# Performance work log

Hardware: AMD Instinct MI355X
Metric: run time of the kernel (lower is better)

Reference implementation:

```python
import jax, jax.numpy as jnp
import numpy as np

N = 50000
E = 800000
H = 128

def _mlp_init(key, sizes, bias_flags):
    ws = []
    for i, (din, dout) in enumerate(zip(sizes[:-1], sizes[1:])):
        key, k1, k2 = jax.random.split(key, 3)
        lim = 1.0 / np.sqrt(din)
        W = jax.random.uniform(k1, (din, dout), jnp.float32, -lim, lim)
        ws.append(W)
        if bias_flags[i]:
            ws.append(jax.random.uniform(k2, (dout,), jnp.float32, -lim, lim))
    return key, ws

def setup_inputs() -> dict:
    key = jax.random.key(0)
    key, kh, kx, ke = jax.random.split(key, 4)
    h = jax.random.normal(kh, (N, H), jnp.float32)
    x = jax.random.normal(kx, (N, 3), jnp.float32)
    edge_index = jax.random.randint(ke, (2, E), 0, N, jnp.int64)
    # edge_mlp: Linear(2H+1, H), Linear(H, H), both with bias
    key, (W_e1, b_e1, W_e2, b_e2) = _mlp_init(key, [2 * H + 1, H, H], [True, True])
    # coord_mlp: Linear(H, H) with bias, Linear(H, 1) no bias
    key, (W_c1, b_c1, W_c2) = _mlp_init(key, [H, H, 1], [True, False])
    # node_mlp: Linear(2H, H), Linear(H, H), both with bias
    key, (W_n1, b_n1, W_n2, b_n2) = _mlp_init(key, [2 * H, H, H], [True, True])
    ln_g = jnp.ones((H,), jnp.float32)
    ln_b = jnp.zeros((H,), jnp.float32)
    return {"h": h, "x": x, "edge_index": edge_index,
            "W_e1": W_e1, "b_e1": b_e1, "W_e2": W_e2, "b_e2": b_e2,
            "W_c1": W_c1, "b_c1": b_c1, "W_c2": W_c2,
            "W_n1": W_n1, "b_n1": b_n1, "W_n2": W_n2, "b_n2": b_n2,
            "ln_g": ln_g, "ln_b": ln_b}

def reference(h, x, edge_index, W_e1, b_e1, W_e2, b_e2, W_c1, b_c1, W_c2,
              W_n1, b_n1, W_n2, b_n2, ln_g, ln_b):
    row, col = edge_index[0], edge_index[1]
    coord_diff = x[row] - x[col]                       # [E, 3]
    dist = jnp.linalg.norm(coord_diff, axis=1, keepdims=True)  # [E, 1]
    radial = dist ** 2
    edge_input = jnp.concatenate([h[row], h[col], radial], axis=1)  # [E, 2H+1]
    m_ij = jax.nn.silu(jax.nn.silu(edge_input @ W_e1 + b_e1) @ W_e2 + b_e2)  # [E, H]
    force_scalar = jnp.tanh(jax.nn.silu(m_ij @ W_c1 + b_c1) @ W_c2) * 0.1    # [E, 1]
    norm_diff = coord_diff / (dist + 1e-8)
    force_vector = norm_diff * force_scalar            # [E, 3]
    x_new = x + jax.ops.segment_sum(force_vector, row, num_segments=N)
    m_i = jax.ops.segment_sum(m_ij, row, num_segments=N)  # [N, H]
    node_input = jnp.concatenate([h, m_i], axis=1)     # [N, 2H]
    h_res = h + jax.nn.silu(node_input @ W_n1 + b_n1) @ W_n2 + b_n2
    mu = jnp.mean(h_res, axis=-1, keepdims=True)
    var = jnp.var(h_res, axis=-1, keepdims=True)
    h_new = (h_res - mu) / jnp.sqrt(var + 1e-5) * ln_g + ln_b
    return (h_new, x_new)
```

## Files before the change

kernel.cpp:

```cpp
#include <hip/hip_runtime.h>
#include <hip/hip_bf16.h>

#define NN 50000
#define NE 800000
#define HH 128
#define SCAN_NB 196

typedef short s16x8 __attribute__((ext_vector_type(8)));
typedef float f32x4 __attribute__((ext_vector_type(4)));
typedef unsigned int u32x4 __attribute__((ext_vector_type(4)));
typedef unsigned int u32x2 __attribute__((ext_vector_type(2)));
typedef __bf16 bf16x2 __attribute__((ext_vector_type(2)));

__device__ __forceinline__ float u2f(unsigned int v) {
    float f;
    __builtin_memcpy(&f, &v, 4);
    return f;
}
__device__ __forceinline__ float bf2f(unsigned short u) {
    return u2f(((unsigned int)u) << 16);
}
__device__ __forceinline__ unsigned short f2bf_sw(float f) {
    unsigned int x;
    __builtin_memcpy(&x, &f, 4);
    unsigned int r = (x + 0x7fffu + ((x >> 16) & 1u)) >> 16;
    return (unsigned short)r;
}
__device__ __forceinline__ unsigned int f2bf_pk(float a, float b) {
#if __has_builtin(__builtin_amdgcn_cvt_pk_bf16_f32)
    bf16x2 p = __builtin_amdgcn_cvt_pk_bf16_f32(a, b);
    unsigned int u;
    __builtin_memcpy(&u, &p, 4);
    return u;
#else
    return (unsigned int)f2bf_sw(a) | ((unsigned int)f2bf_sw(b) << 16);
#endif
}
__device__ __forceinline__ unsigned short f2bf(float a) {
#if __has_builtin(__builtin_amdgcn_cvt_pk_bf16_f32)
    return (unsigned short)(f2bf_pk(a, a) & 0xffffu);
#else
    return f2bf_sw(a);
#endif
}
__device__ __forceinline__ float silu(float v) {
    return v * __builtin_amdgcn_rcpf(1.f + __expf(-v));
}

__global__ void prep_kernel(
    const float* __restrict__ W_e1, const float* __restrict__ W_e2,
    const float* __restrict__ W_c1, const float* __restrict__ W_n1,
    const float* __restrict__ W_n2, const int* __restrict__ eidx,
    unsigned short* __restrict__ PWT, unsigned short* __restrict__ W2T,
    unsigned short* __restrict__ Wc1T, unsigned short* __restrict__ Wn1T,
    unsigned short* __restrict__ Wn2T, int* __restrict__ counts) {
    int idx = blockIdx.x * 256 + threadIdx.x;
    if (idx < 32768) {
        int cp = idx >> 7, k = idx & 127;
        int srow = (cp < 128) ? k : (128 + k);
        PWT[idx] = f2bf(W_e1[srow * 128 + (cp & 127)]);
    } else if (idx < 49152) {
        int i = idx - 32768, n = i >> 7, k = i & 127;
        W2T[i] = f2bf(W_e2[k * 128 + n]);
    } else if (idx < 65536) {
        int i = idx - 49152, n = i >> 7, k = i & 127;
        Wc1T[i] = f2bf(W_c1[k * 128 + n]);
    } else if (idx < 98304) {
        int i = idx - 65536, n = i >> 8, k = i & 255;
        Wn1T[i] = f2bf(W_n1[k * 128 + n]);
    } else if (idx < 114688) {
        int i = idx - 98304, n = i >> 7, k = i & 127;
        Wn2T[i] = f2bf(W_n2[k * 128 + n]);
    } else if (idx < 114688 + NE) {
        int e = idx - 114688;
        int r = eidx[e];
        r = r < 0 ? 0 : (r >= NN ? NN - 1 : r);
        atomicAdd(&counts[r], 1);
    }
}

__global__ void k_partial(const int* __restrict__ counts, int* __restrict__ partials) {
    __shared__ int sm[256];
    int idx = blockIdx.x * 256 + threadIdx.x;
    sm[threadIdx.x] = idx < NN ? counts[idx] : 0;
    __syncthreads();
    for (int s = 128; s > 0; s >>= 1) {
        if (threadIdx.x < s) sm[threadIdx.x] += sm[threadIdx.x + s];
        __syncthreads();
    }
    if (threadIdx.x == 0) partials[blockIdx.x] = sm[0];
}
__global__ void k_scanp(const int* __restrict__ partials, int* __restrict__ scanp) {
    __shared__ int sm[256];
    int t = threadIdx.x;
    int v = t < SCAN_NB ? partials[t] : 0;
    sm[t] = v;
    __syncthreads();
    for (int d = 1; d < 256; d <<= 1) {
        int add = t >= d ? sm[t - d] : 0;
        __syncthreads();
        sm[t] += add;
        __syncthreads();
    }
    scanp[t] = sm[t] - v;
}
__global__ void k_offsets(const int* __restrict__ counts, const int* __restrict__ scanp,
                          int* __restrict__ offsets) {
    __shared__ int sm[256];
    int t = threadIdx.x, idx = blockIdx.x * 256 + t;
    int v = idx < NN ? counts[idx] : 0;
    sm[t] = v;
    __syncthreads();
    for (int d = 1; d < 256; d <<= 1) {
        int add = t >= d ? sm[t - d] : 0;
        __syncthreads();
        sm[t] += add;
        __syncthreads();
    }
    if (idx < NN) offsets[idx] = sm[t] - v + scanp[blockIdx.x];
}

__global__ void k_fill(const int* __restrict__ eidx, const int* __restrict__ offsets,
                       int* __restrict__ cursor, unsigned int* __restrict__ rc) {
    int e = blockIdx.x * 256 + threadIdx.x;
    if (e >= NE) return;
    int r = eidx[e];
    int c = eidx[NE + e];
    r = r < 0 ? 0 : (r >= NN ? NN - 1 : r);
    c = c < 0 ? 0 : (c >= NN ? NN - 1 : c);
    int slot = offsets[r] + atomicAdd(&cursor[r], 1);
    rc[slot] = (unsigned int)r | ((unsigned int)c << 16);
}

__global__ __launch_bounds__(256, 4) void pgemm(
    const float* __restrict__ h, const unsigned short* __restrict__ PWT,
    const float* __restrict__ b1,
    float* __restrict__ P1, unsigned short* __restrict__ P2b) {
    __shared__ unsigned short Alds[64 * 136];
    const int tid = threadIdx.x;
    const int n0 = blockIdx.x * 64;

#pragma unroll
    for (int j = 0; j < 4; j++) {
        int idx = tid + j * 256;
        int e = idx >> 4, ch = idx & 15;
        int node = n0 + e;
        if (node >= NN) node = NN - 1;
        const f32x4* p = (const f32x4*)&h[node * 128 + ch * 8];
        f32x4 a = p[0], b = p[1];
        u32x4 s;
        s[0] = f2bf_pk(a[0], a[1]);
        s[1] = f2bf_pk(a[2], a[3]);
        s[2] = f2bf_pk(b[0], b[1]);
        s[3] = f2bf_pk(b[2], b[3]);
        *(u32x4*)&Alds[e * 136 + ch * 8] = s;
    }
    __syncthreads();

    const int lane = tid & 63;
    const int w = tid >> 6;
    const int ln15 = lane & 15;
    const int q8 = (lane >> 4) * 8, q4 = (lane >> 4) * 4;
    const int cbase = w * 64;

    f32x4 acc[4][4];
#pragma unroll
    for (int et = 0; et < 4; et++)
#pragma unroll
        for (int nt = 0; nt < 4; nt++) acc[et][nt] = (f32x4){0.f, 0.f, 0.f, 0.f};
#pragma unroll
    for (int kk = 0; kk < 4; kk++) {
        int k0 = kk * 32 + q8;
        s16x8 a[4], b[4];
#pragma unroll
        for (int et = 0; et < 4; et++)
            a[et] = *(const s16x8*)&Alds[(et * 16 + ln15) * 136 + k0];
#pragma unroll
        for (int nt = 0; nt < 4; nt++)
            b[nt] = *(const s16x8*)&PWT[(cbase + nt * 16 + ln15) * 128 + k0];
#pragma unroll
        for (int et = 0; et < 4; et++)
#pragma unroll
            for (int nt = 0; nt < 4; nt++)
                acc[et][nt] = __builtin_amdgcn_mfma_f32_16x16x32_bf16(
                    b[nt], a[et], acc[et][nt], 0, 0, 0);
    }
#pragma unroll
    for (int nt = 0; nt < 4; nt++) {
        int cp4 = cbase + nt * 16 + q4;
        bool top = cp4 < 128;
        int col4 = cp4 & 127;
        f32x4 badd = top ? *(const f32x4*)&b1[col4] : (f32x4){0.f, 0.f, 0.f, 0.f};
#pragma unroll
        for (int et = 0; et < 4; et++) {
            int node = n0 + et * 16 + ln15;
            if (node >= NN) node = NN - 1;
            f32x4 v;
#pragma unroll
            for (int r = 0; r < 4; r++) v[r] = acc[et][nt][r] + badd[r];
            if (top) {
                *(f32x4*)&P1[(size_t)node * 128 + col4] = v;
            } else {
                u32x2 s;
                s[0] = f2bf_pk(v[0], v[1]);
                s[1] = f2bf_pk(v[2], v[3]);
                *(u32x2*)&P2b[(size_t)node * 128 + col4] = s;
            }
        }
    }
}

__global__ __launch_bounds__(256, 4) void edge_kernel(
    const float* __restrict__ P1, const unsigned short* __restrict__ P2b,
    const float* __restrict__ x, const unsigned int* __restrict__ rc,
    const float* __restrict__ W1full,
    const unsigned short* __restrict__ W2T, const float* __restrict__ b2,
    const unsigned short* __restrict__ Wc1T, const float* __restrict__ bc1,
    const float* __restrict__ wc2,
    float* __restrict__ m_i, float* __restrict__ x_acc) {
    __shared__ unsigned short mid1[64 * 132];
    __shared__ float wls[128];
    __shared__ float rad[64], ndx[64], ndy[64], ndz[64], fsum[64];
    __shared__ int rowA[64], colA[64];

    const int tid = threadIdx.x;
    const int nwg = NE / 64;
    const int qq = nwg >> 3, r8 = nwg & 7;
    const int xcd = blockIdx.x & 7, pos = blockIdx.x >> 3;
    const int swz = (xcd < r8 ? xcd * (qq + 1) : r8 * (qq + 1) + (xcd - r8) * qq) + pos;
    const int e0 = swz * 64;

    if (tid < 64) {
        unsigned int pk = rc[e0 + tid];
        int r = pk & 0xffff, c = pk >> 16;
        rowA[tid] = r; colA[tid] = c;
        float dx = x[r * 3 + 0] - x[c * 3 + 0];
        float dy = x[r * 3 + 1] - x[c * 3 + 1];
        float dz = x[r * 3 + 2] - x[c * 3 + 2];
        float d2 = dx * dx + dy * dy + dz * dz;
        float dist = sqrtf(d2);
        float inv = __builtin_amdgcn_rcpf(dist + 1e-8f);
        rad[tid] = d2;
        ndx[tid] = dx * inv; ndy[tid] = dy * inv; ndz[tid] = dz * inv;
        fsum[tid] = 0.f;
    } else if (tid >= 128 && tid < 256) {
        int c = tid - 128;
        wls[c] = W1full[256 * 128 + c];
    }
    __syncthreads();

#pragma unroll
    for (int j = 0; j < 4; j++) {
        int idx = tid + j * 256;
        int e = idx >> 4, ch = idx & 15;
        int r = rowA[e], c = colA[e];
        const f32x4* q1 = (const f32x4*)&P1[(size_t)r * 128 + ch * 8];
        f32x4 a0 = q1[0], a1 = q1[1];
        u32x4 c01 = *(const u32x4*)&P2b[(size_t)c * 128 + ch * 8];
        float rd = rad[e];
        int colb = ch * 8;
        u32x4 s;
#pragma unroll
        for (int t = 0; t < 2; t++) {
            float v0 = a0[t * 2]     + u2f(c01[t] << 16)         + rd * wls[colb + t * 2];
            float v1 = a0[t * 2 + 1] + u2f(c01[t] & 0xffff0000u) + rd * wls[colb + t * 2 + 1];
            s[t] = f2bf_pk(silu(v0), silu(v1));
        }
#pragma unroll
        for (int t = 0; t < 2; t++) {
            int cc = colb + 4 + t * 2;
            float v0 = a1[t * 2]     + u2f(c01[t + 2] << 16)         + rd * wls[cc];
            float v1 = a1[t * 2 + 1] + u2f(c01[t + 2] & 0xffff0000u) + rd * wls[cc + 1];
            s[t + 2] = f2bf_pk(silu(v0), silu(v1));
        }
        *(u32x4*)&mid1[e * 132 + colb] = s;
    }
    __syncthreads();

    const int lane = tid & 63;
    const int w = tid >> 6;
    const int ln15 = lane & 15;
    const int q8 = (lane >> 4) * 8, q4 = (lane >> 4) * 4;
    const int nbase = w * 32;

    f32x4 acc[4][2];

#pragma unroll
    for (int et = 0; et < 4; et++)
#pragma unroll
        for (int nt = 0; nt < 2; nt++) acc[et][nt] = (f32x4){0.f, 0.f, 0.f, 0.f};
#pragma unroll
    for (int kk = 0; kk < 4; kk++) {
        int k0 = kk * 32 + q8;
        s16x8 a[4], b[2];
#pragma unroll
        for (int et = 0; et < 4; et++)
            a[et] = *(const s16x8*)&mid1[(et * 16 + ln15) * 132 + k0];
#pragma unroll
        for (int nt = 0; nt < 2; nt++)
            b[nt] = *(const s16x8*)&W2T[(nbase + nt * 16 + ln15) * 128 + k0];
#pragma unroll
        for (int et = 0; et < 4; et++)
#pragma unroll
            for (int nt = 0; nt < 2; nt++)
                acc[et][nt] = __builtin_amdgcn_mfma_f32_16x16x32_bf16(
                    b[nt], a[et], acc[et][nt], 0, 0, 0);
    }
    __syncthreads();
    unsigned short* mid2 = mid1;
#pragma unroll
    for (int et = 0; et < 4; et++) {
        int edge = et * 16 + ln15;
#pragma unroll
        for (int nt = 0; nt < 2; nt++) {
            int colb4 = nbase + nt * 16 + q4;
            f32x4 bias = *(const f32x4*)&b2[colb4];
            u32x2 s;
            s[0] = f2bf_pk(silu(acc[et][nt][0] + bias[0]),
                           silu(acc[et][nt][1] + bias[1]));
            s[1] = f2bf_pk(silu(acc[et][nt][2] + bias[2]),
                           silu(acc[et][nt][3] + bias[3]));
            *(u32x2*)&mid2[edge * 132 + colb4] = s;
        }
    }
    __syncthreads();

#pragma unroll
    for (int et = 0; et < 4; et++)
#pragma unroll
        for (int nt = 0; nt < 2; nt++) acc[et][nt] = (f32x4){0.f, 0.f, 0.f, 0.f};
#pragma unroll
    for (int kk = 0; kk < 4; kk++) {
        int k0 = kk * 32 + q8;
        s16x8 a[4], b[2];
#pragma unroll
        for (int et = 0; et < 4; et++)
            a[et] = *(const s16x8*)&mid2[(et * 16 + ln15) * 132 + k0];
#pragma unroll
        for (int nt = 0; nt < 2; nt++)
            b[nt] = *(const s16x8*)&Wc1T[(nbase + nt * 16 + ln15) * 128 + k0];
#pragma unroll
        for (int et = 0; et < 4; et++)
#pragma unroll
            for (int nt = 0; nt < 2; nt++)
                acc[et][nt] = __builtin_amdgcn_mfma_f32_16x16x32_bf16(
                    b[nt], a[et], acc[et][nt], 0, 0, 0);
    }

    {
        int cp2 = (tid & 63) * 2;
        int g = tid >> 6;
        int r0g = g * 16;
        float a0 = 0.f, a1 = 0.f;
        int cur = rowA[r0g];
        for (int row = r0g; row < r0g + 16; row++) {
            int rn = rowA[row];
            if (rn != cur) {
                atomicAdd(&m_i[(size_t)cur * 128 + cp2], a0);
                atomicAdd(&m_i[(size_t)cur * 128 + cp2 + 1], a1);
                a0 = 0.f; a1 = 0.f;
                cur = rn;
            }
            unsigned int v = *(const unsigned int*)&mid2[row * 132 + cp2];
            a0 += u2f(v << 16);
            a1 += u2f(v & 0xffff0000u);
        }
        atomicAdd(&m_i[(size_t)cur * 128 + cp2], a0);
        atomicAdd(&m_i[(size_t)cur * 128 + cp2 + 1], a1);
    }

    {
#pragma unroll
        for (int et = 0; et < 4; et++) {
            float p = 0.f;
#pragma unroll
            for (int nt = 0; nt < 2; nt++) {
                int colb4 = nbase + nt * 16 + q4;
                f32x4 bias = *(const f32x4*)&bc1[colb4];
                f32x4 w2v  = *(const f32x4*)&wc2[colb4];
#pragma unroll
                for (int r = 0; r < 4; r++)
                    p += silu(acc[et][nt][r] + bias[r]) * w2v[r];
            }
            p += __shfl_xor(p, 16, 64);
            p += __shfl_xor(p, 32, 64);
            if ((lane >> 4) == 0) atomicAdd(&fsum[et * 16 + ln15], p);
        }
    }
    __syncthreads();
    if (tid < 64) {
        float fs = tanhf(fsum[tid]) * 0.1f;
        ndx[tid] *= fs; ndy[tid] *= fs; ndz[tid] *= fs;
    }
    __syncthreads();
    if (tid < 64) {
        bool head = (tid == 0) || (rowA[tid] != rowA[tid - 1]);
        if (head) {
            int rn = rowA[tid];
            float ax = 0.f, ay = 0.f, az = 0.f;
            for (int j = tid; j < 64 && rowA[j] == rn; j++) {
                ax += ndx[j]; ay += ndy[j]; az += ndz[j];
            }
            atomicAdd(&x_acc[rn * 3 + 0], ax);
            atomicAdd(&x_acc[rn * 3 + 1], ay);
            atomicAdd(&x_acc[rn * 3 + 2], az);
        }
    }
}

__global__ __launch_bounds__(256, 4) void node_kernel(
    const float* __restrict__ h, const float* __restrict__ m_i,
    const float* __restrict__ x, const float* __restrict__ x_acc,
    const unsigned short* __restrict__ Wn1T, const float* __restrict__ bn1,
    const unsigned short* __restrict__ Wn2T, const float* __restrict__ bn2,
    const float* __restrict__ ln_g, const float* __restrict__ ln_b,
    float* __restrict__ out_h, float* __restrict__ out_x) {
    __shared__ unsigned short Alds[64 * 264];
    unsigned short* mid1 = Alds;
    float* tile = (float*)Alds;

    const int tid = threadIdx.x;
    const int n0 = blockIdx.x * 64;

    if (tid < 192) {
        int i = n0 * 3 + tid;
        if (i < NN * 3) out_x[i] = x[i] + x_acc[i];
    }

#pragma unroll
    for (int i = 0; i < 8; i++) {
        int idx = tid + i * 256;
        int hr = idx >> 4, ch = idx & 15;
        int e = hr >> 1, half = hr & 1;
        int node = n0 + e;
        if (node >= NN) node = NN - 1;
        const float* src = half ? &m_i[(size_t)node * 128 + ch * 8]
                                : &h[(size_t)node * 128 + ch * 8];
        const f32x4* sp = (const f32x4*)src;
        f32x4 f0 = sp[0], f1 = sp[1];
        u32x4 s;
        s[0] = f2bf_pk(f0[0], f0[1]);
        s[1] = f2bf_pk(f0[2], f0[3]);
        s[2] = f2bf_pk(f1[0], f1[1]);
        s[3] = f2bf_pk(f1[2], f1[3]);
        *(u32x4*)&Alds[e * 264 + half * 128 + ch * 8] = s;
    }
    __syncthreads();

    const int lane = tid & 63;
    const int w = tid >> 6;
    const int ln15 = lane & 15;
    const int q8 = (lane >> 4) * 8, q4 = (lane >> 4) * 4;
    const int nbase = w * 32;

    f32x4 acc[4][2];

#pragma unroll
    for (int et = 0; et < 4; et++)
#pragma unroll
        for (int nt = 0; nt < 2; nt++) acc[et][nt] = (f32x4){0.f, 0.f, 0.f, 0.f};
#pragma unroll
    for (int kk = 0; kk < 8; kk++) {
        int k0 = kk * 32 + q8;
        s16x8 a[4], b[2];
#pragma unroll
        for (int et = 0; et < 4; et++)
            a[et] = *(const s16x8*)&Alds[(et * 16 + ln15) * 264 + k0];
#pragma unroll
        for (int nt = 0; nt < 2; nt++)
            b[nt] = *(const s16x8*)&Wn1T[(nbase + nt * 16 + ln15) * 256 + k0];
#pragma unroll
        for (int et = 0; et < 4; et++)
#pragma unroll
            for (int nt = 0; nt < 2; nt++)
                acc[et][nt] = __builtin_amdgcn_mfma_f32_16x16x32_bf16(
                    b[nt], a[et], acc[et][nt], 0, 0, 0);
    }
    __syncthreads();
#pragma unroll
    for (int et = 0; et < 4; et++) {
        int row = et * 16 + ln15;
#pragma unroll
        for (int nt = 0; nt < 2; nt++) {
            int colb4 = nbase + nt * 16 + q4;
            f32x4 bias = *(const f32x4*)&bn1[colb4];
            u32x2 s;
            s[0] = f2bf_pk(silu(acc[et][nt][0] + bias[0]),
                           silu(acc[et][nt][1] + bias[1]));
            s[1] = f2bf_pk(silu(acc[et][nt][2] + bias[2]),
                           silu(acc[et][nt][3] + bias[3]));
            *(u32x2*)&mid1[row * 132 + colb4] = s;
        }
    }
    __syncthreads();

#pragma unroll
    for (int et = 0; et < 4; et++)
#pragma unroll
        for (int nt = 0; nt < 2; nt++) acc[et][nt] = (f32x4){0.f, 0.f, 0.f, 0.f};
#pragma unroll
    for (int kk = 0; kk < 4; kk++) {
        int k0 = kk * 32 + q8;
        s16x8 a[4], b[2];
#pragma unroll
        for (int et = 0; et < 4; et++)
            a[et] = *(const s16x8*)&mid1[(et * 16 + ln15) * 132 + k0];
#pragma unroll
        for (int nt = 0; nt < 2; nt++)
            b[nt] = *(const s16x8*)&Wn2T[(nbase + nt * 16 + ln15) * 128 + k0];
#pragma unroll
        for (int et = 0; et < 4; et++)
#pragma unroll
            for (int nt = 0; nt < 2; nt++)
                acc[et][nt] = __builtin_amdgcn_mfma_f32_16x16x32_bf16(
                    b[nt], a[et], acc[et][nt], 0, 0, 0);
    }
    __syncthreads();
#pragma unroll
    for (int et = 0; et < 4; et++) {
        int row = et * 16 + ln15;
        int node = n0 + row;
        int nclamp = node >= NN ? NN - 1 : node;
#pragma unroll
        for (int nt = 0; nt < 2; nt++) {
            int colb4 = nbase + nt * 16 + q4;
            f32x4 bias = *(const f32x4*)&bn2[colb4];
            f32x4 hv = *(const f32x4*)&h[(size_t)nclamp * 128 + colb4];
            f32x4 v;
#pragma unroll
            for (int r = 0; r < 4; r++) v[r] = acc[et][nt][r] + bias[r] + hv[r];
            *(f32x4*)&tile[row * 132 + colb4] = v;
        }
    }
    __syncthreads();

    {
        int row = tid >> 2;
        int q = tid & 3;
        float s = 0.f, s2 = 0.f;
#pragma unroll
        for (int c = 0; c < 32; c++) {
            float v = tile[row * 132 + q + c * 4];
            s += v; s2 += v * v;
        }
        s += __shfl_xor(s, 1, 4);  s2 += __shfl_xor(s2, 1, 4);
        s += __shfl_xor(s, 2, 4);  s2 += __shfl_xor(s2, 2, 4);
        float mean = s * (1.f / 128.f);
        float var = s2 * (1.f / 128.f) - mean * mean;
        float rs = rsqrtf(var + 1e-5f);
        int node = n0 + row;
        if (node < NN) {
#pragma unroll
            for (int c = 0; c < 32; c++) {
                int col = q + c * 4;
                float v = (tile[row * 132 + col] - mean) * rs * ln_g[col] + ln_b[col];
                out_h[(size_t)node * 128 + col] = v;
            }
        }
    }
}

extern "C" void kernel_launch(void* const* d_in, const int* in_sizes, int n_in,
                              void* d_out, int out_size, void* d_ws, size_t ws_size,
                              hipStream_t stream) {
    const float* h    = (const float*)d_in[0];
    const float* x    = (const float*)d_in[1];
    const int* eidx   = (const int*)d_in[2];
    const float* W_e1 = (const float*)d_in[3];
    const float* b_e1 = (const float*)d_in[4];
    const float* W_e2 = (const float*)d_in[5];
    const float* b_e2 = (const float*)d_in[6];
    const float* W_c1 = (const float*)d_in[7];
    const float* b_c1 = (const float*)d_in[8];
    const float* W_c2 = (const float*)d_in[9];
    const float* W_n1 = (const float*)d_in[10];
    const float* b_n1 = (const float*)d_in[11];
    const float* W_n2 = (const float*)d_in[12];
    const float* b_n2 = (const float*)d_in[13];
    const float* ln_g = (const float*)d_in[14];
    const float* ln_b = (const float*)d_in[15];

    float* out_h = (float*)d_out;
    float* out_x = out_h + NN * HH;

    char* ws = (char*)d_ws;
    float* m_i    = (float*)ws;
    float* x_acc  = (float*)(ws + 25600000);
    int* counts   = (int*)(ws + 26200000);
    int* cursor   = (int*)(ws + 26400000);
    int* offsets  = (int*)(ws + 26600000);
    int* partials = (int*)(ws + 26800000);
    int* scanp    = (int*)(ws + 26801024);
    unsigned int* rc = (unsigned int*)(ws + 26802048);
    float* P1 = (float*)(ws + 30002048);
    unsigned short* P2b = (unsigned short*)(ws + 55602048);
    unsigned short* PWT  = (unsigned short*)(ws + 81202048);
    unsigned short* W2T  = (unsigned short*)(ws + 81267584);
    unsigned short* Wc1T = (unsigned short*)(ws + 81300352);
    unsigned short* Wn1T = (unsigned short*)(ws + 81333120);
    unsigned short* Wn2T = (unsigned short*)(ws + 81398656);

    hipMemsetAsync(ws, 0, 26800000, stream);

    prep_kernel<<<(114688 + NE + 255) / 256, 256, 0, stream>>>(
        W_e1, W_e2, W_c1, W_n1, W_n2, eidx, PWT, W2T, Wc1T, Wn1T, Wn2T, counts);
    k_partial<<<SCAN_NB, 256, 0, stream>>>(counts, partials);
    k_scanp<<<1, 256, 0, stream>>>(partials, scanp);
    k_offsets<<<SCAN_NB, 256, 0, stream>>>(counts, scanp, offsets);
    k_fill<<<(NE + 255) / 256, 256, 0, stream>>>(eidx, offsets, cursor, rc);
    pgemm<<<(NN + 63) / 64, 256, 0, stream>>>(h, PWT, b_e1, P1, P2b);

    edge_kernel<<<NE / 64, 256, 0, stream>>>(P1, P2b, x, rc, W_e1, W2T, b_e2,
                                             Wc1T, b_c1, W_c2, m_i, x_acc);
    node_kernel<<<(NN + 63) / 64, 256, 0, stream>>>(
        h, m_i, x, x_acc, Wn1T, b_n1, Wn2T, b_n2, ln_g, ln_b, out_h, out_x);
}
```

Baseline: 425.3 us.

## Compute segmented message sums with a one-hot MFMA instead of serial loops

Builds a one-hot segment matrix in shared memory from a ballot over edge rows, then computes per-segment sums of the edge messages with bf16 MFMAs before issuing one atomic per segment and column. This replaces the per-thread serial scan over 16 rows, which flushed atomics whenever the row changed. It also raises wave priority around the MFMA loops. It adds shared-memory use (which may lower occupancy), strided scalar LDS reads to build the B operand, and extra MFMA work.

```diff
diff --git a/kernel.cpp b/kernel.cpp
--- a/kernel.cpp
+++ b/kernel.cpp
@@ -219,9 +219,11 @@
     const float* __restrict__ wc2,
     float* __restrict__ m_i, float* __restrict__ x_acc) {
     __shared__ unsigned short mid1[64 * 132];
+    __shared__ unsigned short Sm[64 * 72];
     __shared__ float wls[128];
     __shared__ float rad[64], ndx[64], ndy[64], ndz[64], fsum[64];
-    __shared__ int rowA[64], colA[64];
+    __shared__ int rowA[64], colA[64], segrow[64];
+    __shared__ int nsegS;
 
     const int tid = threadIdx.x;
     const int nwg = NE / 64;
@@ -230,6 +232,13 @@
     const int swz = (xcd < r8 ? xcd * (qq + 1) : r8 * (qq + 1) + (xcd - r8) * qq) + pos;
     const int e0 = swz * 64;
 
+    {
+        unsigned int* s32 = (unsigned int*)Sm;
+#pragma unroll
+        for (int i = 0; i < 9; i++) s32[tid + i * 256] = 0;
+    }
+
+    int lri_reg = 0;
     if (tid < 64) {
         unsigned int pk = rc[e0 + tid];
         int r = pk & 0xffff, c = pk >> 16;
@@ -243,11 +252,21 @@
         rad[tid] = d2;
         ndx[tid] = dx * inv; ndy[tid] = dy * inv; ndz[tid] = dz * inv;
         fsum[tid] = 0.f;
+        int rprev = __shfl_up(r, 1, 64);
+        bool head = (tid == 0) || (rprev != r);
+        unsigned long long m = __ballot(head);
+        unsigned long long below_incl = ((1ull << tid) << 1) - 1ull;
+        int lri = (int)__popcll(m & below_incl) - 1;
+        lri_reg = lri;
+        if (head) segrow[lri] = r;
+        if (tid == 0) nsegS = (int)__popcll(m);
     } else if (tid >= 128 && tid < 256) {
         int c = tid - 128;
         wls[c] = W1full[256 * 128 + c];
     }
     __syncthreads();
+
+    if (tid < 64) Sm[lri_reg * 72 + tid] = 0x3F80;
 
 #pragma unroll
     for (int j = 0; j < 4; j++) {
@@ -289,6 +308,7 @@
     for (int et = 0; et < 4; et++)
 #pragma unroll
         for (int nt = 0; nt < 2; nt++) acc[et][nt] = (f32x4){0.f, 0.f, 0.f, 0.f};
+    __builtin_amdgcn_s_setprio(1);
 #pragma unroll
     for (int kk = 0; kk < 4; kk++) {
         int k0 = kk * 32 + q8;
@@ -306,6 +326,7 @@
                 acc[et][nt] = __builtin_amdgcn_mfma_f32_16x16x32_bf16(
                     b[nt], a[et], acc[et][nt], 0, 0, 0);
     }
+    __builtin_amdgcn_s_setprio(0);
     __syncthreads();
     unsigned short* mid2 = mid1;
 #pragma unroll
@@ -329,6 +350,7 @@
     for (int et = 0; et < 4; et++)
 #pragma unroll
         for (int nt = 0; nt < 2; nt++) acc[et][nt] = (f32x4){0.f, 0.f, 0.f, 0.f};
+    __builtin_amdgcn_s_setprio(1);
 #pragma unroll
     for (int kk = 0; kk < 4; kk++) {
         int k0 = kk * 32 + q8;
@@ -346,27 +368,53 @@
                 acc[et][nt] = __builtin_amdgcn_mfma_f32_16x16x32_bf16(
                     b[nt], a[et], acc[et][nt], 0, 0, 0);
     }
+    __builtin_amdgcn_s_setprio(0);
 
     {
-        int cp2 = (tid & 63) * 2;
-        int g = tid >> 6;
-        int r0g = g * 16;
-        float a0 = 0.f, a1 = 0.f;
-        int cur = rowA[r0g];
-        for (int row = r0g; row < r0g + 16; row++) {
-            int rn = rowA[row];
-            if (rn != cur) {
-                atomicAdd(&m_i[(size_t)cur * 128 + cp2], a0);
-                atomicAdd(&m_i[(size_t)cur * 128 + cp2 + 1], a1);
-                a0 = 0.f; a1 = 0.f;
-                cur = rn;
+        f32x4 macc[4][2];
+#pragma unroll
+        for (int et = 0; et < 4; et++)
+#pragma unroll
+            for (int nt = 0; nt < 2; nt++) macc[et][nt] = (f32x4){0.f, 0.f, 0.f, 0.f};
+        __builtin_amdgcn_s_setprio(1);
+#pragma unroll
+        for (int kk = 0; kk < 2; kk++) {
+            int k0 = kk * 32 + q8;
+            s16x8 sa[4];
+#pragma unroll
+            for (int et = 0; et < 4; et++)
+                sa[et] = *(const s16x8*)&Sm[(et * 16 + ln15) * 72 + k0];
+            s16x8 mb[2];
+#pragma unroll
+            for (int nt = 0; nt < 2; nt++)
+#pragma unroll
+                for (int j = 0; j < 8; j++)
+                    mb[nt][j] = (short)mid2[(k0 + j) * 132 + nbase + nt * 16 + ln15];
+#pragma unroll
+            for (int et = 0; et < 4; et++)
+#pragma unroll
+                for (int nt = 0; nt < 2; nt++)
+                    macc[et][nt] = __builtin_amdgcn_mfma_f32_16x16x32_bf16(
+                        sa[et], mb[nt], macc[et][nt], 0, 0, 0);
+        }
+        __builtin_amdgcn_s_setprio(0);
+        int nseg = nsegS;
+#pragma unroll
+        for (int et = 0; et < 4; et++) {
+            if (et * 16 + q4 < nseg) {
+#pragma unroll
+                for (int r = 0; r < 4; r++) {
+                    int seg = et * 16 + q4 + r;
+                    if (seg < nseg) {
+                        int rn = segrow[seg];
+#pragma unroll
+                        for (int nt = 0; nt < 2; nt++)
+                            atomicAdd(&m_i[(size_t)rn * 128 + nbase + nt * 16 + ln15],
+                                      macc[et][nt][r]);
+                    }
+                }
             }
-            unsigned int v = *(const unsigned int*)&mid2[row * 132 + cp2];
-            a0 += u2f(v << 16);
-            a1 += u2f(v & 0xffff0000u);
-        }
-        atomicAdd(&m_i[(size_t)cur * 128 + cp2], a0);
-        atomicAdd(&m_i[(size_t)cur * 128 + cp2 + 1], a1);
+        }
     }
 
     {
```

Result: slower. 471.7 us (+10.9%).
